# Kernel optimization log

Measured on AMD Instinct MI355X. Metric: run time of the kernel, lower is better.

The kernel has to match this reference:

```python
import jax, jax.numpy as jnp
import numpy as np
import math

E = 256          # embed_dims
H = 8            # num_heads
ITER = 2         # iterative steps
PC_RANGE = (-140.8, -40.0, -3.0, 140.8, 40.0, 1.0)


def sine_embed(pos, num_feats):
    # pos: (..., 3) in (0,1); returns (..., 3*num_feats), per-coord interleaved sin/cos
    scale = 2.0 * math.pi
    i = jnp.arange(num_feats, dtype=jnp.float32)
    dim_t = 10000.0 ** (2.0 * jnp.floor(i / 2.0) / num_feats)
    p = pos[..., None] * scale / dim_t                      # (..., 3, F)
    emb = jnp.stack([jnp.sin(p[..., 0::2]), jnp.cos(p[..., 1::2])], axis=-1)
    emb = emb.reshape(p.shape[:-1] + (num_feats,))          # (..., 3, F)
    return emb.reshape(pos.shape[:-1] + (3 * num_feats,))


def mha(q, k, v, Wi, bi, Wo, bo, n_heads):
    # torch nn.MultiheadAttention math, seq-first layout: q (L,N,C), k/v (M,N,C)
    L, N, C = q.shape
    D = C // n_heads
    qp = (q @ Wi[:C].T + bi[:C]).reshape(L, N, n_heads, D)
    kp = (k @ Wi[C:2 * C].T + bi[C:2 * C]).reshape(k.shape[0], N, n_heads, D)
    vp = (v @ Wi[2 * C:].T + bi[2 * C:]).reshape(v.shape[0], N, n_heads, D)
    scores = jnp.einsum('lnhd,mnhd->nhlm', qp, kp) / math.sqrt(D)
    attn = jax.nn.softmax(scores, axis=-1)
    o = jnp.einsum('nhlm,mnhd->lnhd', attn, vp).reshape(L, N, C)
    return o @ Wo.T + bo


def setup_inputs() -> dict:
    key = jax.random.key(0)
    ks = jax.random.split(key, 12)
    Q, TOT, B, LMAX = 2048, 40, 8, 5
    s = 0.02
    return {
        'x': jax.random.normal(ks[0], (Q, TOT, E), jnp.float32),
        'reference_points': jax.random.uniform(ks[1], (TOT, Q, 3), jnp.float32),
        'pairwise_t_matrix': jax.random.normal(ks[2], (B, LMAX, LMAX, 4, 4), jnp.float32),
        'record_len': np.full((B,), 5, dtype=np.int64),
        'in_proj_w': jax.random.normal(ks[3], (3 * E, E), jnp.float32) * s,
        'in_proj_b': jnp.zeros((3 * E,), jnp.float32),
        'out_w': jax.random.normal(ks[4], (E, E), jnp.float32) * s,
        'out_b': jnp.zeros((E,), jnp.float32),
        'bev_w1': jax.random.normal(ks[5], (E, 3 * E), jnp.float32) * s,
        'bev_b1': jnp.zeros((E,), jnp.float32),
        'bev_w2': jax.random.normal(ks[6], (E, E), jnp.float32) * s,
        'bev_b2': jnp.zeros((E,), jnp.float32),
    }


def reference(x, reference_points, pairwise_t_matrix, in_proj_w, in_proj_b,
              out_w, out_b, bev_w1, bev_b1, bev_w2, bev_b2, record_len):
    rl = np.asarray(record_len)
    offsets = np.concatenate([[0], np.cumsum(rl)]).astype(int)
    lo = jnp.asarray(PC_RANGE[:3], jnp.float32)
    hi = jnp.asarray(PC_RANGE[3:], jnp.float32)

    x_cav = jnp.transpose(x, (1, 0, 2))                    # (total_cav, Q, C)
    ref = reference_points * (hi - lo) + lo                # un-normalize to pc_range

    outs = []
    for b in range(len(rl)):
        s, e = offsets[b], offsets[b + 1]
        n = e - s
        b_x = x_cav[s:e]                                   # (n, Q, C)
        if n == 1:
            outs.append(b_x)
            continue
        b_ref = ref[s:e]                                   # (n, Q, 3)
        t_ego = pairwise_t_matrix[b, :n, 0]                # (n, 4, 4) transform-to-ego
        homo = jnp.concatenate([b_ref, jnp.ones(b_ref.shape[:-1] + (1,), b_ref.dtype)], axis=-1)
        trans = jax.nn.sigmoid(jnp.einsum('nij,nqj->nqi', t_ego, homo)[..., :3])
        pe = sine_embed(trans, E)                          # (n, Q, 3E)
        bev = jax.nn.relu(pe @ bev_w1.T + bev_b1) @ bev_w2.T + bev_b2  # (n, Q, C)

        ego = b_x[0:1]
        neigh = b_x[1:]                                    # (n-1, Q, C)
        kk = neigh + bev[1:]
        for _ in range(ITER):
            q = jnp.broadcast_to(ego, neigh.shape)
            o = q + mha(q, kk, neigh, in_proj_w, in_proj_b, out_w, out_b, H)
            ego = jnp.sum(o, axis=0, keepdims=True)
        outs.append(jnp.concatenate([ego, neigh], axis=0))

    out = jnp.concatenate(outs, axis=0)                    # (total_cav, Q, C)
    return jnp.transpose(out, (1, 0, 2))                   # (Q, total_cav, C)
```

## Files before the change

kernel.cpp:

```cpp
#include <hip/hip_runtime.h>
#include <cstdint>
#include <cstddef>

typedef __bf16 bf16;
typedef __attribute__((ext_vector_type(8))) __bf16 bf16x8;
typedef __attribute__((ext_vector_type(4))) float f32x4;
typedef __attribute__((ext_vector_type(4))) unsigned int u32x4;

#define QN 2048

#if __has_builtin(__builtin_amdgcn_sinf)
#define SIN_REV(x) __builtin_amdgcn_sinf(x)
#define COS_REV(x) __builtin_amdgcn_cosf(x)
#else
#define SIN_REV(x) __sinf((x) * 6.283185307179586f)
#define COS_REV(x) __cosf((x) * 6.283185307179586f)
#endif

__device__ __forceinline__ float sigmoidf_(float v) { return 1.0f / (1.0f + __expf(-v)); }

__device__ __forceinline__ bf16x8 cvt8(const float* p) {
  const f32x4* p4 = (const f32x4*)p;
  f32x4 lo = p4[0], hi = p4[1];
  bf16x8 r;
#pragma unroll
  for (int j = 0; j < 4; ++j) { r[j] = (bf16)lo[j]; r[j + 4] = (bf16)hi[j]; }
  return r;
}

__device__ __forceinline__ void load_lds16(const bf16* g, bf16* l) {
  __builtin_amdgcn_global_load_lds(
      (const __attribute__((address_space(1))) void*)g,
      (__attribute__((address_space(3))) void*)l, 16, 0, 0);
}

__global__ __launch_bounds__(256) void copy_ker(const u32x4* __restrict__ in,
                                                u32x4* __restrict__ out, int n) {
  int i = blockIdx.x * 256 + threadIdx.x;
  if (i >= n) return;
  int t = (i >> 6) % 40;
  if ((t % 5) == 0) return;
  out[i] = in[i];
}

__global__ __launch_bounds__(256) void cvtw_ker(const float* __restrict__ ipw,
                                                const float* __restrict__ ow,
                                                const float* __restrict__ w1,
                                                bf16* __restrict__ wb) {
  int e = (blockIdx.x * 256 + threadIdx.x) * 8;
  const float* src; int off;
  if (e < 196608)      { src = ipw; off = e; }
  else if (e < 262144) { src = ow;  off = e - 196608; }
  else                 { src = w1;  off = e - 262144; }
  *(bf16x8*)(wb + e) = cvt8(src + off);
}

__global__ __launch_bounds__(256) void wcomb_ker(const float* __restrict__ ipw,
                                                 const float* __restrict__ ipb,
                                                 const float* __restrict__ w2f,
                                                 const float* __restrict__ b2f,
                                                 bf16* __restrict__ Wc,
                                                 float* __restrict__ bkf) {
  __shared__ float row[256];
  __shared__ float red[256];
  const int j = blockIdx.x, l = threadIdx.x;
  row[l] = ipw[65536 + j * 256 + l];
  __syncthreads();
  float acc = 0.f;
#pragma unroll 4
  for (int m = 0; m < 256; ++m) acc += row[m] * w2f[m * 256 + l];
  Wc[(size_t)j * 512 + l] = (bf16)acc;
  Wc[(size_t)j * 512 + 256 + l] = (bf16)row[l];
  red[l] = row[l] * b2f[l];
  __syncthreads();
  for (int s = 128; s > 0; s >>= 1) {
    if (l < s) red[l] += red[l + s];
    __syncthreads();
  }
  if (l == 0) bkf[j] = ipb[256 + j] + red[0];
}

template <int AMODE, int EPI, int KDIM>
__global__ __launch_bounds__(256) void gemm_ker(
    const bf16* __restrict__ A, const bf16* __restrict__ W,
    const float* __restrict__ bias, const float* __restrict__ x,
    const float* __restrict__ rp, const float* __restrict__ pm,
    bf16* __restrict__ outB) {
  __shared__ bf16 As[128][40];
  __shared__ bf16 Bs[128][32];

  const int tid = threadIdx.x;
  const int bidm = blockIdx.x >> 1;
  const int bidn = blockIdx.x & 1;
  const int rowBase = bidm << 7;
  const int colBase = bidn << 7;

  const int wave = tid >> 6, lane = tid & 63;
  const int m16 = lane & 15, quad = lane >> 4;
  const int wr = wave >> 1, wc = wave & 1;

  const int sRow = tid >> 1, sHalf = tid & 1;
  const int rgA = rowBase + sRow;

  const float* afp = nullptr;
  float tr0 = 0.f, tr1 = 0.f, tr2 = 0.f;
  if constexpr (AMODE == 1) {
    int b = rgA >> 13, j = (rgA >> 11) & 3, q = rgA & 2047;
    int t = b * 5 + 1 + j;
    const float* rpp = rp + ((size_t)t * QN + q) * 3;
    float r0 = rpp[0] * 281.6f - 140.8f;
    float r1 = rpp[1] * 80.0f - 40.0f;
    float r2 = rpp[2] * 4.0f - 3.0f;
    const float* T = pm + (size_t)t * 80;
    tr0 = sigmoidf_(T[0] * r0 + T[1] * r1 + T[2] * r2 + T[3]);
    tr1 = sigmoidf_(T[4] * r0 + T[5] * r1 + T[6] * r2 + T[7]);
    tr2 = sigmoidf_(T[8] * r0 + T[9] * r1 + T[10] * r2 + T[11]);
  } else if constexpr (AMODE == 2 || AMODE == 5) {
    int b = rgA >> 13, j = (rgA >> 11) & 3, q = rgA & 2047;
    afp = x + (((size_t)q * 40 + b * 5 + 1 + j) << 8);
  }

  const bf16* wsrc = W + (size_t)(colBase + (wave << 5) + (lane >> 2)) * KDIM + ((lane & 3) << 3);
  bf16* bdst0 = &Bs[(wave << 5)][0];
  bf16* bdst1 = &Bs[(wave << 5) + 16][0];

  f32x4 acc[4][4] = {};

  for (int k0 = 0; k0 < KDIM; k0 += 32) {
    load_lds16(wsrc + k0, bdst0);
    load_lds16(wsrc + (size_t)16 * KDIM + k0, bdst1);

    bf16x8 a0, a1;
    if constexpr (AMODE == 1) {
      int c = k0 >> 8;
      float tc = (c == 0) ? tr0 : (c == 1 ? tr1 : tr2);
      int ti0 = ((k0 & 255) + (sHalf << 4)) >> 1;
      float freq = exp2f((float)ti0 * -0.10381025296522975f);
#pragma unroll
      for (int p = 0; p < 4; ++p) {
        float ang = tc * freq;
        a0[2 * p]     = (bf16)SIN_REV(ang);
        a0[2 * p + 1] = (bf16)COS_REV(ang);
        freq *= 0.93057204092467f;
      }
#pragma unroll
      for (int p = 0; p < 4; ++p) {
        float ang = tc * freq;
        a1[2 * p]     = (bf16)SIN_REV(ang);
        a1[2 * p + 1] = (bf16)COS_REV(ang);
        freq *= 0.93057204092467f;
      }
    } else if constexpr (AMODE == 0) {
      const bf16* ap = A + (size_t)rgA * KDIM + k0 + (sHalf << 4);
      a0 = ((const bf16x8*)ap)[0];
      a1 = ((const bf16x8*)ap)[1];
    } else if constexpr (AMODE == 5) {
      if (k0 < 256) {
        const bf16* ap = A + ((size_t)rgA << 8) + k0 + (sHalf << 4);
        a0 = ((const bf16x8*)ap)[0];
        a1 = ((const bf16x8*)ap)[1];
      } else {
        const float* fp = afp + (k0 - 256) + (sHalf << 4);
        a0 = cvt8(fp);
        a1 = cvt8(fp + 8);
      }
    } else {
      const float* fp = afp + k0 + (sHalf << 4);
      a0 = cvt8(fp);
      a1 = cvt8(fp + 8);
    }
    *(bf16x8*)(&As[sRow][sHalf << 4]) = a0;
    *(bf16x8*)(&As[sRow][(sHalf << 4) + 8]) = a1;
    __syncthreads();

    bf16x8 afr[4], bfr[4];
#pragma unroll
    for (int mt = 0; mt < 4; ++mt)
      afr[mt] = *(const bf16x8*)(&As[(wr << 6) + (mt << 4) + m16][quad << 3]);
#pragma unroll
    for (int nt = 0; nt < 4; ++nt)
      bfr[nt] = *(const bf16x8*)(&Bs[(wc << 6) + (nt << 4) + m16][quad << 3]);
#pragma unroll
    for (int mt = 0; mt < 4; ++mt)
#pragma unroll
      for (int nt = 0; nt < 4; ++nt)
        acc[mt][nt] = __builtin_amdgcn_mfma_f32_16x16x32_bf16(
            afr[mt], bfr[nt], acc[mt][nt], 0, 0, 0);
    __syncthreads();
  }

#pragma unroll
  for (int mt = 0; mt < 4; ++mt) {
#pragma unroll
    for (int nt = 0; nt < 4; ++nt) {
      const int col = colBase + (wc << 6) + (nt << 4) + m16;
      const float bv = bias[col];
#pragma unroll
      for (int rg = 0; rg < 4; ++rg) {
        const int r = rowBase + (wr << 6) + (mt << 4) + (quad << 2) + rg;
        float v = acc[mt][nt][rg] + bv;
        if constexpr (EPI == 0) {
          outB[(size_t)r * 256 + col] = (bf16)fmaxf(v, 0.0f);
        } else {
          outB[(size_t)r * 256 + col] = (bf16)v;
        }
      }
    }
  }
}

__device__ __forceinline__ void proj32db(const bf16 (*AP)[256],
                                         bf16 (*BsP)[256][32],
                                         const bf16* __restrict__ WB,
                                         f32x4 (*acc)[4], int wave, int lane) {
  const int m16 = lane & 15, quad = lane >> 4;
#define PSTAGE(P_, K_)                                                        \
  { _Pragma("unroll") for (int i_ = 0; i_ < 4; ++i_) {                        \
      const bf16* src_ = WB +                                                 \
          (size_t)((wave << 6) + (i_ << 4) + (lane >> 2)) * 256 + (K_) +      \
          ((lane & 3) << 3);                                                  \
      load_lds16(src_, &BsP[P_][(wave << 6) + (i_ << 4)][0]); } }
  PSTAGE(0, 0);
#pragma unroll
  for (int t = 0; t < 8; ++t) {
    const int p = t & 1;
    if (t < 7) {
      PSTAGE(p ^ 1, (t + 1) << 5);
      asm volatile("s_waitcnt vmcnt(4)" ::: "memory");
    } else {
      asm volatile("s_waitcnt vmcnt(0)" ::: "memory");
    }
    __builtin_amdgcn_sched_barrier(0);
    const int k0 = t << 5;
    bf16x8 afr[2], bfr[4];
#pragma unroll
    for (int mt = 0; mt < 2; ++mt) {
      const int r = (mt << 4) + m16;
      afr[mt] = *(const bf16x8*)(&AP[r][(((k0 >> 3) + quad) ^ (r & 7)) << 3]);
    }
#pragma unroll
    for (int nt = 0; nt < 4; ++nt)
      bfr[nt] = *(const bf16x8*)(&BsP[p][(wave << 6) + (nt << 4) + m16][quad << 3]);
#pragma unroll
    for (int mt = 0; mt < 2; ++mt)
#pragma unroll
      for (int nt = 0; nt < 4; ++nt)
        acc[mt][nt] = __builtin_amdgcn_mfma_f32_16x16x32_bf16(
            afr[mt], bfr[nt], acc[mt][nt], 0, 0, 0);
  }
#undef PSTAGE
}

__device__ __forceinline__ void attn_phase(bf16 (*P)[256],
                                           const bf16* __restrict__ kp,
                                           const bf16* __restrict__ vp,
                                           int rowBase, int tid) {
  const int r = tid >> 3, h = tid & 7;
  const int re = rowBase + r, b = re >> 11, q = re & 2047;
  float qv[32];
#pragma unroll
  for (int i = 0; i < 4; ++i) {
    bf16x8 t = *(const bf16x8*)(&P[r][((((h << 2) + i)) ^ (r & 7)) << 3]);
#pragma unroll
    for (int j = 0; j < 8; ++j) qv[i * 8 + j] = (float)t[j];
  }
  const size_t base = ((size_t)(b * 4) * QN + q) * 256 + h * 32;
  float s[4];
#pragma unroll
  for (int m = 0; m < 4; ++m) {
    const bf16x8* kv = (const bf16x8*)(kp + base + (size_t)m * (QN * 256));
    float a = 0.f;
#pragma unroll
    for (int i = 0; i < 4; ++i) {
      bf16x8 t = kv[i];
#pragma unroll
      for (int j = 0; j < 8; ++j) a += qv[i * 8 + j] * (float)t[j];
    }
    s[m] = a * 0.17677669529663687f;
  }
  float mx = fmaxf(fmaxf(s[0], s[1]), fmaxf(s[2], s[3]));
  float e0 = __expf(s[0] - mx), e1 = __expf(s[1] - mx);
  float e2 = __expf(s[2] - mx), e3 = __expf(s[3] - mx);
  float inv = 1.0f / (e0 + e1 + e2 + e3);
  float w[4] = {e0 * inv, e1 * inv, e2 * inv, e3 * inv};
  float ov[32] = {};
#pragma unroll
  for (int m = 0; m < 4; ++m) {
    const bf16x8* vv = (const bf16x8*)(vp + base + (size_t)m * (QN * 256));
#pragma unroll
    for (int i = 0; i < 4; ++i) {
      bf16x8 t = vv[i];
#pragma unroll
      for (int j = 0; j < 8; ++j) ov[i * 8 + j] += w[m] * (float)t[j];
    }
  }
#pragma unroll
  for (int i = 0; i < 4; ++i) {
    bf16x8 t;
#pragma unroll
    for (int j = 0; j < 8; ++j) t[j] = (bf16)ov[i * 8 + j];
    *(bf16x8*)(&P[r][((((h << 2) + i)) ^ (r & 7)) << 3]) = t;
  }
}

__global__ __launch_bounds__(256, 2) void iter_ker(
    const bf16* __restrict__ kp, const bf16* __restrict__ vp,
    const bf16* __restrict__ wq, const bf16* __restrict__ owb,
    const float* __restrict__ qb, const float* __restrict__ ob,
    const float* __restrict__ x, float* __restrict__ out) {
  __shared__ bf16 P1[32][256];
  __shared__ bf16 P2[32][256];
  __shared__ bf16 Bs[2][256][32];

  const int tid = threadIdx.x;
  const int rowBase = blockIdx.x << 5;
  const int wave = tid >> 6, lane = tid & 63;
  const int m16 = lane & 15, quad = lane >> 4;

  {
    const int r = tid >> 3, e = tid & 7;
    const int re = rowBase + r, b = re >> 11, q = re & 2047;
    const float* src = x + (((size_t)q * 40 + b * 5) << 8) + (e << 5);
#pragma unroll
    for (int s = 0; s < 4; ++s) {
      bf16x8 v = cvt8(src + s * 8);
      *(bf16x8*)(&P1[r][((((e << 2) + s)) ^ (r & 7)) << 3]) = v;
    }
  }
  __syncthreads();

  float e1r[2][4][4];
  f32x4 acc[2][4];

#define ZACC                                                                  \
  { _Pragma("unroll") for (int mt = 0; mt < 2; ++mt)                          \
    _Pragma("unroll") for (int nt = 0; nt < 4; ++nt) {                        \
      f32x4 z = {0.f, 0.f, 0.f, 0.f}; acc[mt][nt] = z; } }

#define QEPI                                                                  \
  { _Pragma("unroll") for (int mt = 0; mt < 2; ++mt)                          \
    _Pragma("unroll") for (int nt = 0; nt < 4; ++nt) {                        \
      const int col = (wave << 6) + (nt << 4) + m16;                          \
      const float bv = qb[col];                                               \
      _Pragma("unroll") for (int rg = 0; rg < 4; ++rg) {                      \
        const int row = (mt << 4) + (quad << 2) + rg;                         \
        P2[row][(((col >> 3) ^ (row & 7)) << 3) + (col & 7)] =                \
            (bf16)(acc[mt][nt][rg] + bv);                                     \
      } } }

  ZACC;
  proj32db(P1, Bs, wq, acc, wave, lane);
  QEPI;
  __syncthreads();
  attn_phase(P2, kp, vp, rowBase, tid);
  __syncthreads();
  ZACC;
  proj32db(P2, Bs, owb, acc, wave, lane);
#pragma unroll
  for (int mt = 0; mt < 2; ++mt)
#pragma unroll
    for (int nt = 0; nt < 4; ++nt) {
      const int col = (wave << 6) + (nt << 4) + m16;
      const float bv = ob[col];
#pragma unroll
      for (int rg = 0; rg < 4; ++rg) {
        const int row = (mt << 4) + (quad << 2) + rg;
        const int re = rowBase + row, b = re >> 11, q = re & 2047;
        float xe = x[(((size_t)q * 40 + b * 5) << 8) + col];
        float e1 = 4.0f * (xe + acc[mt][nt][rg] + bv);
        e1r[mt][nt][rg] = e1;
        P1[row][(((col >> 3) ^ (row & 7)) << 3) + (col & 7)] = (bf16)e1;
      }
    }
  __syncthreads();

  ZACC;
  proj32db(P1, Bs, wq, acc, wave, lane);
  QEPI;
  __syncthreads();
  attn_phase(P2, kp, vp, rowBase, tid);
  __syncthreads();
  ZACC;
  proj32db(P2, Bs, owb, acc, wave, lane);
#pragma unroll
  for (int mt = 0; mt < 2; ++mt)
#pragma unroll
    for (int nt = 0; nt < 4; ++nt) {
      const int col = (wave << 6) + (nt << 4) + m16;
      const float bv = ob[col];
#pragma unroll
      for (int rg = 0; rg < 4; ++rg) {
        const int row = (mt << 4) + (quad << 2) + rg;
        const int re = rowBase + row, b = re >> 11, q = re & 2047;
        out[(((size_t)q * 40 + b * 5) << 8) + col] =
            4.0f * (e1r[mt][nt][rg] + acc[mt][nt][rg] + bv);
      }
    }
#undef ZACC
#undef QEPI
}

extern "C" void kernel_launch(void* const* d_in, const int* in_sizes, int n_in,
                              void* d_out, int out_size, void* d_ws, size_t ws_size,
                              hipStream_t stream) {
  (void)n_in; (void)out_size; (void)ws_size;
  const float* x   = (const float*)d_in[0];
  const float* rp  = (const float*)d_in[1];
  const float* pm  = (const float*)d_in[2];
  const int wbase = (in_sizes[3] == 8) ? 4 : 3;
  const float* ipw = (const float*)d_in[wbase + 0];
  const float* ipb = (const float*)d_in[wbase + 1];
  const float* ow  = (const float*)d_in[wbase + 2];
  const float* obv = (const float*)d_in[wbase + 3];
  const float* w1  = (const float*)d_in[wbase + 4];
  const float* b1  = (const float*)d_in[wbase + 5];
  const float* w2  = (const float*)d_in[wbase + 6];
  const float* b2  = (const float*)d_in[wbase + 7];
  float* out = (float*)d_out;
  char* ws = (char*)d_ws;

  bf16* h    = (bf16*)(ws + 0);
  bf16* kp   = (bf16*)(ws + 33554432);
  bf16* vp   = (bf16*)(ws + 67108864);
  bf16* wb   = (bf16*)(ws + 100663296);
  bf16* Wc   = (bf16*)(ws + 101711872);
  float* bkf = (float*)(ws + 101974016);
  const bf16* wq  = wb;
  const bf16* wv  = wb + 131072;
  const bf16* owb = wb + 196608;
  const bf16* w1b = wb + 262144;

  cvtw_ker<<<224, 256, 0, stream>>>(ipw, ow, w1, wb);
  wcomb_ker<<<256, 256, 0, stream>>>(ipw, ipb, w2, b2, Wc, bkf);
  copy_ker<<<20480, 256, 0, stream>>>((const u32x4*)x, (u32x4*)out, 5242880);
  gemm_ker<1, 0, 768><<<1024, 256, 0, stream>>>(nullptr, w1b, b1, x, rp, pm, h);
  gemm_ker<5, 2, 512><<<1024, 256, 0, stream>>>(h, Wc, bkf, x, rp, pm, kp);
  gemm_ker<2, 2, 256><<<1024, 256, 0, stream>>>(nullptr, wv, ipb + 512, x, rp, pm, vp);
  iter_ker<<<512, 256, 0, stream>>>(kp, vp, wq, owb, ipb, obv, x, out);
}
```

Before: 368.3 us.

## Double-buffer LDS tiles in gemm kernel to overlap loads with MFMA

Converts the GEMM main loop to a two-stage software pipeline. The A and B LDS tiles are double-buffered, and the next K-slice's global-to-LDS B load and A register prep (loads, conversion or sine embedding) are issued before the current slice's MFMAs. This drops one barrier per iteration and hides memory and transcendental latency behind compute. In exchange it doubles LDS use and holds the prefetched A registers across the MFMA block, which could reduce occupancy.

```diff
diff --git a/kernel.cpp b/kernel.cpp
--- a/kernel.cpp
+++ b/kernel.cpp
@@ -86,8 +86,9 @@
     const float* __restrict__ bias, const float* __restrict__ x,
     const float* __restrict__ rp, const float* __restrict__ pm,
     bf16* __restrict__ outB) {
-  __shared__ bf16 As[128][40];
-  __shared__ bf16 Bs[128][32];
+  __shared__ bf16 As[2][128][40];
+  __shared__ bf16 Bs[2][128][32];
+  constexpr int NS = KDIM / 32;
 
   const int tid = threadIdx.x;
   const int bidm = blockIdx.x >> 1;
@@ -121,73 +122,86 @@
   }
 
   const bf16* wsrc = W + (size_t)(colBase + (wave << 5) + (lane >> 2)) * KDIM + ((lane & 3) << 3);
-  bf16* bdst0 = &Bs[(wave << 5)][0];
-  bf16* bdst1 = &Bs[(wave << 5) + 16][0];
 
   f32x4 acc[4][4] = {};
-
-  for (int k0 = 0; k0 < KDIM; k0 += 32) {
-    load_lds16(wsrc + k0, bdst0);
-    load_lds16(wsrc + (size_t)16 * KDIM + k0, bdst1);
-
-    bf16x8 a0, a1;
-    if constexpr (AMODE == 1) {
-      int c = k0 >> 8;
-      float tc = (c == 0) ? tr0 : (c == 1 ? tr1 : tr2);
-      int ti0 = ((k0 & 255) + (sHalf << 4)) >> 1;
-      float freq = exp2f((float)ti0 * -0.10381025296522975f);
-#pragma unroll
-      for (int p = 0; p < 4; ++p) {
-        float ang = tc * freq;
-        a0[2 * p]     = (bf16)SIN_REV(ang);
-        a0[2 * p + 1] = (bf16)COS_REV(ang);
-        freq *= 0.93057204092467f;
-      }
-#pragma unroll
-      for (int p = 0; p < 4; ++p) {
-        float ang = tc * freq;
-        a1[2 * p]     = (bf16)SIN_REV(ang);
-        a1[2 * p + 1] = (bf16)COS_REV(ang);
-        freq *= 0.93057204092467f;
-      }
-    } else if constexpr (AMODE == 0) {
-      const bf16* ap = A + (size_t)rgA * KDIM + k0 + (sHalf << 4);
-      a0 = ((const bf16x8*)ap)[0];
-      a1 = ((const bf16x8*)ap)[1];
-    } else if constexpr (AMODE == 5) {
-      if (k0 < 256) {
-        const bf16* ap = A + ((size_t)rgA << 8) + k0 + (sHalf << 4);
-        a0 = ((const bf16x8*)ap)[0];
-        a1 = ((const bf16x8*)ap)[1];
-      } else {
-        const float* fp = afp + (k0 - 256) + (sHalf << 4);
-        a0 = cvt8(fp);
-        a1 = cvt8(fp + 8);
-      }
-    } else {
-      const float* fp = afp + k0 + (sHalf << 4);
-      a0 = cvt8(fp);
-      a1 = cvt8(fp + 8);
-    }
-    *(bf16x8*)(&As[sRow][sHalf << 4]) = a0;
-    *(bf16x8*)(&As[sRow][(sHalf << 4) + 8]) = a1;
-    __syncthreads();
-
+  bf16x8 a0, a1;
+
+#define STAGE_B(P_, K_)                                                       \
+  { load_lds16(wsrc + (K_), &Bs[P_][(wave << 5)][0]);                         \
+    load_lds16(wsrc + (size_t)16 * KDIM + (K_), &Bs[P_][(wave << 5) + 16][0]); }
+
+#define PREP_A(K_)                                                            \
+  if constexpr (AMODE == 1) {                                                 \
+    int c_ = (K_) >> 8;                                                       \
+    float tc_ = (c_ == 0) ? tr0 : (c_ == 1 ? tr1 : tr2);                      \
+    int ti0_ = (((K_) & 255) + (sHalf << 4)) >> 1;                            \
+    float freq_ = exp2f((float)ti0_ * -0.10381025296522975f);                 \
+    _Pragma("unroll") for (int p_ = 0; p_ < 4; ++p_) {                        \
+      float ang_ = tc_ * freq_;                                               \
+      a0[2 * p_] = (bf16)SIN_REV(ang_);                                       \
+      a0[2 * p_ + 1] = (bf16)COS_REV(ang_);                                   \
+      freq_ *= 0.93057204092467f;                                             \
+    }                                                                         \
+    _Pragma("unroll") for (int p_ = 0; p_ < 4; ++p_) {                        \
+      float ang_ = tc_ * freq_;                                               \
+      a1[2 * p_] = (bf16)SIN_REV(ang_);                                       \
+      a1[2 * p_ + 1] = (bf16)COS_REV(ang_);                                   \
+      freq_ *= 0.93057204092467f;                                             \
+    }                                                                         \
+  } else if constexpr (AMODE == 0) {                                          \
+    const bf16* ap_ = A + (size_t)rgA * KDIM + (K_) + (sHalf << 4);           \
+    a0 = ((const bf16x8*)ap_)[0];                                             \
+    a1 = ((const bf16x8*)ap_)[1];                                             \
+  } else if constexpr (AMODE == 5) {                                          \
+    if ((K_) < 256) {                                                         \
+      const bf16* ap_ = A + ((size_t)rgA << 8) + (K_) + (sHalf << 4);         \
+      a0 = ((const bf16x8*)ap_)[0];                                           \
+      a1 = ((const bf16x8*)ap_)[1];                                           \
+    } else {                                                                  \
+      const float* fp_ = afp + (K_) - 256 + (sHalf << 4);                     \
+      a0 = cvt8(fp_);                                                         \
+      a1 = cvt8(fp_ + 8);                                                     \
+    }                                                                         \
+  } else {                                                                    \
+    const float* fp_ = afp + (K_) + (sHalf << 4);                             \
+    a0 = cvt8(fp_);                                                           \
+    a1 = cvt8(fp_ + 8);                                                       \
+  }
+
+#define WRITE_A(P_)                                                           \
+  { *(bf16x8*)(&As[P_][sRow][sHalf << 4]) = a0;                               \
+    *(bf16x8*)(&As[P_][sRow][(sHalf << 4) + 8]) = a1; }
+
+  STAGE_B(0, 0);
+  PREP_A(0);
+  WRITE_A(0);
+  __syncthreads();
+
+  for (int t = 0; t < NS; ++t) {
+    const int p = t & 1;
+    if (t + 1 < NS) {
+      STAGE_B(p ^ 1, (t + 1) << 5);
+      PREP_A((t + 1) << 5);
+    }
     bf16x8 afr[4], bfr[4];
 #pragma unroll
     for (int mt = 0; mt < 4; ++mt)
-      afr[mt] = *(const bf16x8*)(&As[(wr << 6) + (mt << 4) + m16][quad << 3]);
+      afr[mt] = *(const bf16x8*)(&As[p][(wr << 6) + (mt << 4) + m16][quad << 3]);
 #pragma unroll
     for (int nt = 0; nt < 4; ++nt)
-      bfr[nt] = *(const bf16x8*)(&Bs[(wc << 6) + (nt << 4) + m16][quad << 3]);
+      bfr[nt] = *(const bf16x8*)(&Bs[p][(wc << 6) + (nt << 4) + m16][quad << 3]);
 #pragma unroll
     for (int mt = 0; mt < 4; ++mt)
 #pragma unroll
       for (int nt = 0; nt < 4; ++nt)
         acc[mt][nt] = __builtin_amdgcn_mfma_f32_16x16x32_bf16(
             afr[mt], bfr[nt], acc[mt][nt], 0, 0, 0);
+    if (t + 1 < NS) WRITE_A(p ^ 1);
     __syncthreads();
   }
+#undef STAGE_B
+#undef PREP_A
+#undef WRITE_A
 
 #pragma unroll
   for (int mt = 0; mt < 4; ++mt) {
```

New measurement: 370.4 us. Within noise of the previous version (+0.6%).
